# Performance work log

Measured on AMD Instinct MI355X. Metric: run time of the kernel, lower is better.

Reference implementation:

```python
import jax, jax.numpy as jnp
import numpy as np

N = 100000   # num_nodes
E = 1250000  # num_edges
IN = 64
HID = 64
OUT = 64
LN_EPS = 1e-5


def _gcn_conv(x, src, dst, W, b, n):
    # PyG GCNConv: add self-loops, symmetric deg^{-1/2} normalization, then linear.
    h = x @ W  # (N, out)
    deg = jax.ops.segment_sum(jnp.ones(src.shape[0], h.dtype), dst, num_segments=n) + 1.0  # +1 self-loop
    dinv = jax.lax.rsqrt(deg)
    norm = dinv[src] * dinv[dst]  # (E,)
    out = jax.ops.segment_sum(h[src] * norm[:, None], dst, num_segments=n)
    out = out + h * (dinv * dinv)[:, None]  # self-loop message
    return out + b


def _sage_conv(x, src, dst, Wl, bl, Wr, n):
    # PyG SAGEConv(aggr='mean'): lin_l(mean_{j in N(i)} x_j) + lin_r(x_i); bias only in lin_l.
    cnt = jax.ops.segment_sum(jnp.ones(src.shape[0], x.dtype), dst, num_segments=n)
    agg = jax.ops.segment_sum(x[src], dst, num_segments=n) / jnp.maximum(cnt, 1.0)[:, None]
    return agg @ Wl + bl + x @ Wr


def _layer_norm(x, g, b):
    mu = jnp.mean(x, axis=-1, keepdims=True)
    var = jnp.var(x, axis=-1, keepdims=True)
    return (x - mu) * jax.lax.rsqrt(var + LN_EPS) * g + b


def setup_inputs() -> dict:
    key = jax.random.key(0)
    ks = jax.random.split(key, 16)
    def w(k, shape):
        fan_in = shape[0]
        return (jax.random.normal(k, shape, jnp.float32) / np.sqrt(fan_in)).astype(jnp.float32)
    x = jax.random.normal(ks[0], (N, IN), jnp.float32)
    edge_index = jax.random.randint(ks[1], (2, E), 0, N, dtype=jnp.int64)
    return {
        "x": x,
        "edge_index": edge_index,
        "gcn_w1": w(ks[2], (IN, HID)), "gcn_b1": jnp.zeros((HID,), jnp.float32),
        "gcn_w2": w(ks[3], (HID, OUT)), "gcn_b2": jnp.zeros((OUT,), jnp.float32),
        "sage_wl1": w(ks[4], (IN, HID)), "sage_bl1": jnp.zeros((HID,), jnp.float32),
        "sage_wr1": w(ks[5], (IN, HID)),
        "sage_wl2": w(ks[6], (HID, OUT)), "sage_bl2": jnp.zeros((OUT,), jnp.float32),
        "sage_wr2": w(ks[7], (HID, OUT)),
        "gcn_ln_g": jnp.ones((OUT,), jnp.float32), "gcn_ln_b": jnp.zeros((OUT,), jnp.float32),
        "sage_ln_g": jnp.ones((OUT,), jnp.float32), "sage_ln_b": jnp.zeros((OUT,), jnp.float32),
        "proj_w": w(ks[8], (2 * OUT, OUT)), "proj_b": jnp.zeros((OUT,), jnp.float32),
    }


def reference(x, edge_index, gcn_w1, gcn_b1, gcn_w2, gcn_b2,
              sage_wl1, sage_bl1, sage_wr1, sage_wl2, sage_bl2, sage_wr2,
              gcn_ln_g, gcn_ln_b, sage_ln_g, sage_ln_b, proj_w, proj_b):
    src, dst = edge_index[0], edge_index[1]
    n = x.shape[0]
    # GCN branch (dropout p=0 / eval -> identity)
    g = jax.nn.relu(_gcn_conv(x, src, dst, gcn_w1, gcn_b1, n))
    g = _gcn_conv(g, src, dst, gcn_w2, gcn_b2, n)
    # SAGE branch
    s = jax.nn.relu(_sage_conv(x, src, dst, sage_wl1, sage_bl1, sage_wr1, n))
    s = _sage_conv(s, src, dst, sage_wl2, sage_bl2, sage_wr2, n)
    # Norm + projected-concat fusion
    g = _layer_norm(g, gcn_ln_g, gcn_ln_b)
    s = _layer_norm(s, sage_ln_g, sage_ln_b)
    cat = jnp.concatenate([g, s], axis=-1)  # (N, 2*OUT)
    return cat @ proj_w + proj_b
```

## Files before the change

### kernel.cpp

```cpp
#include <hip/hip_runtime.h>


#define SCAN_CHUNK 2048

typedef __attribute__((ext_vector_type(8))) short short8;
typedef __attribute__((ext_vector_type(4))) short short4v;
typedef __attribute__((ext_vector_type(4))) float floatx4;

__device__ __forceinline__ unsigned short f2bf(float f) {
    unsigned int u = __float_as_uint(f);
    unsigned int r = u + 0x7FFFu + ((u >> 16) & 1u);
    return (unsigned short)(r >> 16);
}
__device__ __forceinline__ float bf2f(unsigned short h) {
    return __uint_as_float(((unsigned int)h) << 16);
}

__device__ __forceinline__ unsigned lds_addr(const void* p) {
    return (unsigned)(unsigned long long)(__attribute__((address_space(3))) const char*)p;
}

__device__ __forceinline__ short8 cat44(short4v lo, short4v hi) {
    short8 r;
    r[0] = lo[0]; r[1] = lo[1]; r[2] = lo[2]; r[3] = lo[3];
    r[4] = hi[0]; r[5] = hi[1]; r[6] = hi[2]; r[7] = hi[3];
    return r;
}

template<int NF, int CTB>
__device__ __forceinline__ void tr_read4(unsigned a0, short8 bf[4]) {
    short4v l0, h0, l1, h1, l2, h2, l3, h3;
    asm volatile(
        "ds_read_b64_tr_b16 %0, %8 offset:%9\n\t"
        "ds_read_b64_tr_b16 %1, %8 offset:%10\n\t"
        "ds_read_b64_tr_b16 %2, %8 offset:%11\n\t"
        "ds_read_b64_tr_b16 %3, %8 offset:%12\n\t"
        "ds_read_b64_tr_b16 %4, %8 offset:%13\n\t"
        "ds_read_b64_tr_b16 %5, %8 offset:%14\n\t"
        "ds_read_b64_tr_b16 %6, %8 offset:%15\n\t"
        "ds_read_b64_tr_b16 %7, %8 offset:%16\n\t"
        "s_waitcnt lgkmcnt(0)"
        : "=&v"(l0), "=&v"(h0), "=&v"(l1), "=&v"(h1),
          "=&v"(l2), "=&v"(h2), "=&v"(l3), "=&v"(h3)
        : "v"(a0),
          "i"((0 * NF + CTB + 0) * 128), "i"((1 * NF + CTB + 0) * 128),
          "i"((0 * NF + CTB + 1) * 128), "i"((1 * NF + CTB + 1) * 128),
          "i"((0 * NF + CTB + 2) * 128), "i"((1 * NF + CTB + 2) * 128),
          "i"((0 * NF + CTB + 3) * 128), "i"((1 * NF + CTB + 3) * 128)
        : "memory");
    bf[0] = cat44(l0, h0);
    bf[1] = cat44(l1, h1);
    bf[2] = cat44(l2, h2);
    bf[3] = cat44(l3, h3);
}

__global__ void k_count(const int* __restrict__ ei, int E, int* __restrict__ cnt,
                        int* __restrict__ rank) {
    int i = blockIdx.x * blockDim.x + threadIdx.x;
    int e = i * 4;
    if (e + 4 <= E) {
        int4 d = *(const int4*)&ei[E + e];
        int4 r;
        r.x = atomicAdd(&cnt[d.x], 1);
        r.y = atomicAdd(&cnt[d.y], 1);
        r.z = atomicAdd(&cnt[d.z], 1);
        r.w = atomicAdd(&cnt[d.w], 1);
        *(int4*)&rank[e] = r;
    } else {
        for (int j = e; j < E; ++j) rank[j] = atomicAdd(&cnt[ei[E + j]], 1);
    }
}

__global__ void k_scan_reduce(const int* __restrict__ cnt, int N, int* __restrict__ blockSums) {
    __shared__ int lds[256];
    int base = blockIdx.x * SCAN_CHUNK;
    int t = threadIdx.x;
    int s = 0;
    for (int j = 0; j < 8; ++j) {
        int idx = base + t * 8 + j;
        if (idx < N) s += cnt[idx] + 1;
    }
    lds[t] = s;
    __syncthreads();
    for (int d = 128; d > 0; d >>= 1) {
        if (t < d) lds[t] += lds[t + d];
        __syncthreads();
    }
    if (t == 0) blockSums[blockIdx.x] = lds[0];
}

__global__ void k_scan_spine(int* __restrict__ blockSums, int B) {
    if (threadIdx.x == 0 && blockIdx.x == 0) {
        int run = 0;
        for (int b = 0; b < B; ++b) { int v = blockSums[b]; blockSums[b] = run; run += v; }
    }
}

__global__ void k_scan_write(const int* __restrict__ cnt, int N,
                             const int* __restrict__ blockSums,
                             int* __restrict__ offs, float* __restrict__ dinv) {
    __shared__ int lds[256];
    int base = blockIdx.x * SCAN_CHUNK;
    int t = threadIdx.x;
    int v[8];
    int s = 0;
    for (int j = 0; j < 8; ++j) {
        int idx = base + t * 8 + j;
        v[j] = (idx < N) ? cnt[idx] : 0;
        s += (idx < N) ? v[j] + 1 : 0;
    }
    lds[t] = s;
    __syncthreads();
    for (int d = 1; d < 256; d <<= 1) {
        int x = (t >= d) ? lds[t - d] : 0;
        __syncthreads();
        lds[t] += x;
        __syncthreads();
    }
    int excl = (t == 0) ? 0 : lds[t - 1];
    int run = blockSums[blockIdx.x] + excl;
    for (int j = 0; j < 8; ++j) {
        int idx = base + t * 8 + j;
        if (idx < N) {
            offs[idx] = run;
            run += v[j] + 1;
            dinv[idx] = rsqrtf((float)v[j] + 1.0f);
            if (idx == N - 1) offs[N] = run;
        }
    }
}

__global__ void k_fill(const int* __restrict__ ei, int E, const int* __restrict__ offs,
                       const int* __restrict__ rank, const float* __restrict__ dinv,
                       int* __restrict__ csr, unsigned int* __restrict__ pk, int use_pk) {
    int i = blockIdx.x * blockDim.x + threadIdx.x;
    int e = i * 4;
    if (e + 4 <= E) {
        int4 s = *(const int4*)&ei[e];
        int4 d = *(const int4*)&ei[E + e];
        int4 r = *(const int4*)&rank[e];
        int p0 = offs[d.x] + r.x, p1 = offs[d.y] + r.y;
        int p2 = offs[d.z] + r.z, p3 = offs[d.w] + r.w;
        csr[p0] = s.x; csr[p1] = s.y; csr[p2] = s.z; csr[p3] = s.w;
        if (use_pk) {
            pk[p0] = ((unsigned)(d.x & 15) << 16) | f2bf(dinv[s.x] * dinv[d.x]);
            pk[p1] = ((unsigned)(d.y & 15) << 16) | f2bf(dinv[s.y] * dinv[d.y]);
            pk[p2] = ((unsigned)(d.z & 15) << 16) | f2bf(dinv[s.z] * dinv[d.z]);
            pk[p3] = ((unsigned)(d.w & 15) << 16) | f2bf(dinv[s.w] * dinv[d.w]);
        }
    } else {
        for (int j = e; j < E; ++j) {
            int dd = ei[E + j];
            int p = offs[dd] + rank[j];
            csr[p] = ei[j];
            if (use_pk) pk[p] = ((unsigned)(dd & 15) << 16) | f2bf(dinv[ei[j]] * dinv[dd]);
        }
    }
}

__global__ void k_self(const int* __restrict__ offs, const int* __restrict__ cnt,
                       const float* __restrict__ dinv,
                       int* __restrict__ csr, unsigned int* __restrict__ pk, int N) {
    int i = blockIdx.x * blockDim.x + threadIdx.x;
    if (i < N) {
        int pos = offs[i] + cnt[i];
        float di = dinv[i];
        csr[pos] = i;
        pk[pos] = ((unsigned)(i & 15) << 16) | (1u << 20) | f2bf(di * di);
    }
}

__global__ void k_xtobf16(const float* __restrict__ x, unsigned short* __restrict__ xb, int total) {
    int i = blockIdx.x * blockDim.x + threadIdx.x;
    int e = i * 8;
    if (e + 8 <= total) {
        float4 a = *(const float4*)&x[e];
        float4 b = *(const float4*)&x[e + 4];
        short8 o;
        o[0] = (short)f2bf(a.x); o[1] = (short)f2bf(a.y);
        o[2] = (short)f2bf(a.z); o[3] = (short)f2bf(a.w);
        o[4] = (short)f2bf(b.x); o[5] = (short)f2bf(b.y);
        o[6] = (short)f2bf(b.z); o[7] = (short)f2bf(b.w);
        *(short8*)&xb[e] = o;
    } else {
        for (int j = e; j < total; ++j) xb[j] = f2bf(x[j]);
    }
}

template<int ROWSH>
__launch_bounds__(256)
__global__ void k_gatherM(const unsigned short* __restrict__ feat,
                          const int* __restrict__ csr,
                          const unsigned int* __restrict__ pk,
                          const int* __restrict__ offs, const int* __restrict__ cnt,
                          unsigned short* __restrict__ agg, int N) {
    constexpr int NF = ROWSH / 16;
    constexpr int EPP = (NF == 8) ? 4 : 8;
    constexpr int PASSES = 32 / EPP;

    __shared__ unsigned short sbuf[4 * 32 * ROWSH];

    const int lane = threadIdx.x & 63;
    const int wave = threadIdx.x >> 6;
    const int base = blockIdx.x * 64 + wave * 16;
    if (base >= N) return;

    unsigned short* wb = &sbuf[wave * 32 * ROWSH];
    const unsigned wboff = lds_addr(wb);
    const int q = lane >> 4;
    const int d16 = lane & 15;

    const int parity = lane & 1;
    const int ei_low = (lane >> 1) & 3;
    const int sf_sub = (lane >> 3) & (NF - 1);
    const int ei_high = (NF == 8) ? 0 : (lane >> 5);
    const int ei = ei_high * 4 + ei_low;
    const int sf = sf_sub * 16 + parity * 8;

    const int elo = offs[base];
    const int ehi = offs[min(base + 16, N)];

    floatx4 accg[4], accs[4];
#pragma unroll
    for (int i = 0; i < 4; ++i) {
        accg[i] = floatx4{0.f, 0.f, 0.f, 0.f};
        accs[i] = floatx4{0.f, 0.f, 0.f, 0.f};
    }

    const unsigned a0 = wboff + (unsigned)(q * 2 * NF) * 128u + (unsigned)d16 * 8u;

    if (elo < ehi) {
        const int emax = ehi - 1;

        auto meta = [&](int k0, int& csrv, unsigned& pkv) {
            int idx = k0 + lane;
            int idc = idx <= emax ? idx : emax;
            csrv = csr[idc];
            pkv = (idx < ehi) ? pk[idx] : 0x00100000u;
        };
        auto issue = [&](short8* stg, int csrv) {
#pragma unroll
            for (int p = 0; p < PASSES; ++p) {
                int src = __shfl(csrv, p * EPP + ei, 64);
                stg[p] = *(const short8*)&feat[(size_t)src * ROWSH + sf];
            }
        };
        auto process = [&](const short8* stg, unsigned pkv) {
#pragma unroll
            for (int p = 0; p < PASSES; ++p)
                *(short8*)&wb[p * 512 + lane * 8] = stg[p];
            short8 aG, aS;
#pragma unroll
            for (int j = 0; j < 8; ++j) {
                unsigned u = (unsigned)__shfl((int)pkv, q * 8 + j, 64);
                unsigned hi = u >> 16;
                bool match = (int)(hi & 15u) == d16;
                aG[j] = match ? (short)(u & 0xFFFFu) : (short)0;
                aS[j] = (match && !(hi & 16u)) ? (short)0x3F80 : (short)0;
            }
            asm volatile("s_waitcnt lgkmcnt(0)" ::: "memory");
            __builtin_amdgcn_sched_barrier(0);
            short8 bG[4];
            tr_read4<NF, 0>(a0, bG);
#pragma unroll
            for (int ct = 0; ct < 4; ++ct)
                accg[ct] = __builtin_amdgcn_mfma_f32_16x16x32_bf16(aG, bG[ct], accg[ct], 0, 0, 0);
            if constexpr (NF == 8) {
                short8 bS[4];
                tr_read4<NF, 4>(a0, bS);
#pragma unroll
                for (int ct = 0; ct < 4; ++ct)
                    accs[ct] = __builtin_amdgcn_mfma_f32_16x16x32_bf16(aS, bS[ct], accs[ct], 0, 0, 0);
            } else {
#pragma unroll
                for (int ct = 0; ct < 4; ++ct)
                    accs[ct] = __builtin_amdgcn_mfma_f32_16x16x32_bf16(aS, bG[ct], accs[ct], 0, 0, 0);
            }
        };

        int csrvA, csrvN;
        unsigned pkvA, pkvB, pkvN;
        short8 sA[PASSES], sB[PASSES];

        meta(elo, csrvA, pkvA);
        issue(sA, csrvA);
        meta(elo + 32, csrvN, pkvN);

        int k0 = elo;
        while (true) {
            issue(sB, csrvN);
            pkvB = pkvN;
            meta(k0 + 64, csrvN, pkvN);
            process(sA, pkvA);
            k0 += 32;
            if (k0 >= ehi) break;
            issue(sA, csrvN);
            pkvA = pkvN;
            meta(k0 + 64, csrvN, pkvN);
            process(sB, pkvB);
            k0 += 32;
            if (k0 >= ehi) break;
        }
    }

#pragma unroll
    for (int r = 0; r < 4; ++r) {
        int node = base + q * 4 + r;
        if (node < N) {
            float rn = 1.0f / fmaxf((float)cnt[node], 1.0f);
#pragma unroll
            for (int ct = 0; ct < 4; ++ct) {
                agg[(size_t)node * 128 + ct * 16 + d16]      = f2bf(accg[ct][r]);
                agg[(size_t)node * 128 + 64 + ct * 16 + d16] = f2bf(accs[ct][r] * rn);
            }
        }
    }
}

__device__ __forceinline__ void xor_reduce8(float4& a, float4& b) {
    a.x += __shfl_xor(a.x, 16, 64); a.y += __shfl_xor(a.y, 16, 64);
    a.z += __shfl_xor(a.z, 16, 64); a.w += __shfl_xor(a.w, 16, 64);
    b.x += __shfl_xor(b.x, 16, 64); b.y += __shfl_xor(b.y, 16, 64);
    b.z += __shfl_xor(b.z, 16, 64); b.w += __shfl_xor(b.w, 16, 64);
    a.x += __shfl_xor(a.x, 32, 64); a.y += __shfl_xor(a.y, 32, 64);
    a.z += __shfl_xor(a.z, 32, 64); a.w += __shfl_xor(a.w, 32, 64);
    b.x += __shfl_xor(b.x, 32, 64); b.y += __shfl_xor(b.y, 32, 64);
    b.z += __shfl_xor(b.z, 32, 64); b.w += __shfl_xor(b.w, 32, 64);
}

__device__ __forceinline__ float red16(float v) {
    v += __shfl_xor(v, 1, 64);
    v += __shfl_xor(v, 2, 64);
    v += __shfl_xor(v, 4, 64);
    v += __shfl_xor(v, 8, 64);
    return v;
}

__global__ void k_gather1_f32(const float* __restrict__ x, const int* __restrict__ csr,
                              const int* __restrict__ offs, const int* __restrict__ cnt,
                              const float* __restrict__ dinv,
                              unsigned short* __restrict__ agg, int N) {
    int lane = threadIdx.x & 63;
    int wave = threadIdx.x >> 6;
    int node = blockIdx.x * 4 + wave;
    if (node >= N) return;
    int c = lane & 15, grp = lane >> 4;

    int st = offs[node];
    int cn = cnt[node];
    float di = dinv[node];

    float4 aA = {0.f, 0.f, 0.f, 0.f}, aB = {0.f, 0.f, 0.f, 0.f};
    for (int e = 0; e < cn; e += 8) {
        int i0 = e + grp, i1 = e + 4 + grp;
        float m0 = (i0 < cn) ? 1.f : 0.f;
        float m1 = (i1 < cn) ? 1.f : 0.f;
        int s0 = csr[st + (i0 < cn ? i0 : cn - 1)];
        int s1 = csr[st + (i1 < cn ? i1 : cn - 1)];
        float w0 = m0 * dinv[s0];
        float w1 = m1 * dinv[s1];
        float4 v0 = *(const float4*)&x[(size_t)s0 * 64 + 4 * c];
        float4 v1 = *(const float4*)&x[(size_t)s1 * 64 + 4 * c];
        aA.x += w0 * v0.x + w1 * v1.x; aA.y += w0 * v0.y + w1 * v1.y;
        aA.z += w0 * v0.z + w1 * v1.z; aA.w += w0 * v0.w + w1 * v1.w;
        aB.x += m0 * v0.x + m1 * v1.x; aB.y += m0 * v0.y + m1 * v1.y;
        aB.z += m0 * v0.z + m1 * v1.z; aB.w += m0 * v0.w + m1 * v1.w;
    }
    xor_reduce8(aA, aB);

    if (grp == 0) {
        float4 sq = *(const float4*)&x[(size_t)node * 64 + 4 * c];
        float d2 = di * di;
        ushort4 o;
        o.x = f2bf(di * aA.x + d2 * sq.x); o.y = f2bf(di * aA.y + d2 * sq.y);
        o.z = f2bf(di * aA.z + d2 * sq.z); o.w = f2bf(di * aA.w + d2 * sq.w);
        *(ushort4*)&agg[(size_t)node * 128 + 4 * c] = o;
    } else if (grp == 1) {
        float rn = 1.0f / fmaxf((float)cn, 1.0f);
        ushort4 o;
        o.x = f2bf(aB.x * rn); o.y = f2bf(aB.y * rn);
        o.z = f2bf(aB.z * rn); o.w = f2bf(aB.w * rn);
        *(ushort4*)&agg[(size_t)node * 128 + 64 + 4 * c] = o;
    }
}

__global__ void k_gather2(const unsigned short* __restrict__ gs, const int* __restrict__ csr,
                          const int* __restrict__ offs, const int* __restrict__ cnt,
                          const float* __restrict__ dinv,
                          unsigned short* __restrict__ agg, int N) {
    int lane = threadIdx.x & 63;
    int wave = threadIdx.x >> 6;
    int node = blockIdx.x * 4 + wave;
    if (node >= N) return;
    int c = lane & 15, grp = lane >> 4;

    int st = offs[node];
    int cn = cnt[node];
    float di = dinv[node];

    float4 aC = {0.f, 0.f, 0.f, 0.f}, aD = {0.f, 0.f, 0.f, 0.f};
    for (int e = 0; e < cn; e += 8) {
        int i0 = e + grp, i1 = e + 4 + grp;
        float m0 = (i0 < cn) ? 1.f : 0.f;
        float m1 = (i1 < cn) ? 1.f : 0.f;
        int s0 = csr[st + (i0 < cn ? i0 : cn - 1)];
        int s1 = csr[st + (i1 < cn ? i1 : cn - 1)];
        float w0 = m0 * dinv[s0];
        float w1 = m1 * dinv[s1];
        const unsigned short* p0 = gs + (size_t)s0 * 128 + 4 * c;
        const unsigned short* p1 = gs + (size_t)s1 * 128 + 4 * c;
        ushort4 g0u = *(const ushort4*)p0;
        ushort4 g1u = *(const ushort4*)p1;
        ushort4 t0u = *(const ushort4*)(p0 + 64);
        ushort4 t1u = *(const ushort4*)(p1 + 64);
        aC.x += w0 * bf2f(g0u.x) + w1 * bf2f(g1u.x);
        aC.y += w0 * bf2f(g0u.y) + w1 * bf2f(g1u.y);
        aC.z += w0 * bf2f(g0u.z) + w1 * bf2f(g1u.z);
        aC.w += w0 * bf2f(g0u.w) + w1 * bf2f(g1u.w);
        aD.x += m0 * bf2f(t0u.x) + m1 * bf2f(t1u.x);
        aD.y += m0 * bf2f(t0u.y) + m1 * bf2f(t1u.y);
        aD.z += m0 * bf2f(t0u.z) + m1 * bf2f(t1u.z);
        aD.w += m0 * bf2f(t0u.w) + m1 * bf2f(t1u.w);
    }
    xor_reduce8(aC, aD);

    if (grp == 0) {
        ushort4 su = *(const ushort4*)&gs[(size_t)node * 128 + 4 * c];
        float d2 = di * di;
        ushort4 o;
        o.x = f2bf(di * aC.x + d2 * bf2f(su.x));
        o.y = f2bf(di * aC.y + d2 * bf2f(su.y));
        o.z = f2bf(di * aC.z + d2 * bf2f(su.z));
        o.w = f2bf(di * aC.w + d2 * bf2f(su.w));
        *(ushort4*)&agg[(size_t)node * 128 + 4 * c] = o;
    } else if (grp == 1) {
        float rn = 1.0f / fmaxf((float)cn, 1.0f);
        ushort4 o;
        o.x = f2bf(aD.x * rn); o.y = f2bf(aD.y * rn);
        o.z = f2bf(aD.z * rn); o.w = f2bf(aD.w * rn);
        *(ushort4*)&agg[(size_t)node * 128 + 64 + 4 * c] = o;
    }
}

__launch_bounds__(512, 1)
__global__ void k_gemm1(const unsigned short* __restrict__ agg,
                        const unsigned short* __restrict__ xb,
                        const float* __restrict__ xf, int use_xb,
                        const float* __restrict__ W1, const float* __restrict__ b1,
                        const float* __restrict__ Wl1, const float* __restrict__ bl1,
                        const float* __restrict__ Wr1,
                        unsigned short* __restrict__ buf1, int N) {
    alignas(16) __shared__ unsigned short sW[3][4096];
    int t = threadIdx.x;
    for (int i = t; i < 1536; i += 512) {
        int m = i >> 9;
        int rem = i & 511;
        int f = rem >> 6;
        int L = rem & 63;
        int kb = (f >> 2) * 32 + (L >> 4) * 8;
        int o = (f & 3) * 16 + (L & 15);
        const float* Wsrc = (m == 0) ? W1 : (m == 1) ? Wl1 : Wr1;
        unsigned short* dst = &sW[m][f * 512 + L * 8];
        #pragma unroll
        for (int j = 0; j < 8; ++j) dst[j] = f2bf(Wsrc[(kb + j) * 64 + o]);
    }
    __syncthreads();

    int lane = t & 63;
    int wave = t >> 6;
    int quad = lane >> 4;
    int n16 = lane & 15;
    int base = blockIdx.x * 128 + wave * 16;
    if (base >= N) return;

    int nm = base + n16;
    if (nm >= N) nm = N - 1;
    const unsigned short* ar = agg + (size_t)nm * 128;

    {
        short8 a0 = *(const short8*)(ar + quad * 8);
        short8 a1 = *(const short8*)(ar + 32 + quad * 8);
        floatx4 g0 = {0.f, 0.f, 0.f, 0.f}, g1 = g0, g2 = g0, g3 = g0;
        g0 = __builtin_amdgcn_mfma_f32_16x16x32_bf16(a0, *(const short8*)&sW[0][0 * 512 + lane * 8], g0, 0, 0, 0);
        g0 = __builtin_amdgcn_mfma_f32_16x16x32_bf16(a1, *(const short8*)&sW[0][4 * 512 + lane * 8], g0, 0, 0, 0);
        g1 = __builtin_amdgcn_mfma_f32_16x16x32_bf16(a0, *(const short8*)&sW[0][1 * 512 + lane * 8], g1, 0, 0, 0);
        g1 = __builtin_amdgcn_mfma_f32_16x16x32_bf16(a1, *(const short8*)&sW[0][5 * 512 + lane * 8], g1, 0, 0, 0);
        g2 = __builtin_amdgcn_mfma_f32_16x16x32_bf16(a0, *(const short8*)&sW[0][2 * 512 + lane * 8], g2, 0, 0, 0);
        g2 = __builtin_amdgcn_mfma_f32_16x16x32_bf16(a1, *(const short8*)&sW[0][6 * 512 + lane * 8], g2, 0, 0, 0);
        g3 = __builtin_amdgcn_mfma_f32_16x16x32_bf16(a0, *(const short8*)&sW[0][3 * 512 + lane * 8], g3, 0, 0, 0);
        g3 = __builtin_amdgcn_mfma_f32_16x16x32_bf16(a1, *(const short8*)&sW[0][7 * 512 + lane * 8], g3, 0, 0, 0);
        floatx4 gt[4] = {g0, g1, g2, g3};
        #pragma unroll
        for (int nt = 0; nt < 4; ++nt) {
            float bg = b1[nt * 16 + n16];
            #pragma unroll
            for (int r = 0; r < 4; ++r) {
                int node = base + quad * 4 + r;
                if (node < N)
                    buf1[(size_t)node * 128 + nt * 16 + n16] = f2bf(fmaxf(gt[nt][r] + bg, 0.f));
            }
        }
    }

    {
        short8 a0 = *(const short8*)(ar + 64 + quad * 8);
        short8 a1 = *(const short8*)(ar + 96 + quad * 8);
        short8 ax0, ax1;
        if (use_xb) {
            ax0 = *(const short8*)&xb[(size_t)nm * 64 + quad * 8];
            ax1 = *(const short8*)&xb[(size_t)nm * 64 + 32 + quad * 8];
        } else {
            float4 xq0 = *(const float4*)&xf[(size_t)nm * 64 + quad * 8];
            float4 xq1 = *(const float4*)&xf[(size_t)nm * 64 + quad * 8 + 4];
            float4 xq2 = *(const float4*)&xf[(size_t)nm * 64 + 32 + quad * 8];
            float4 xq3 = *(const float4*)&xf[(size_t)nm * 64 + 32 + quad * 8 + 4];
            ax0[0] = (short)f2bf(xq0.x); ax0[1] = (short)f2bf(xq0.y);
            ax0[2] = (short)f2bf(xq0.z); ax0[3] = (short)f2bf(xq0.w);
            ax0[4] = (short)f2bf(xq1.x); ax0[5] = (short)f2bf(xq1.y);
            ax0[6] = (short)f2bf(xq1.z); ax0[7] = (short)f2bf(xq1.w);
            ax1[0] = (short)f2bf(xq2.x); ax1[1] = (short)f2bf(xq2.y);
            ax1[2] = (short)f2bf(xq2.z); ax1[3] = (short)f2bf(xq2.w);
            ax1[4] = (short)f2bf(xq3.x); ax1[5] = (short)f2bf(xq3.y);
            ax1[6] = (short)f2bf(xq3.z); ax1[7] = (short)f2bf(xq3.w);
        }

        floatx4 s0 = {0.f, 0.f, 0.f, 0.f}, s1 = s0, s2 = s0, s3 = s0;
        s0 = __builtin_amdgcn_mfma_f32_16x16x32_bf16(a0, *(const short8*)&sW[1][0 * 512 + lane * 8], s0, 0, 0, 0);
        s0 = __builtin_amdgcn_mfma_f32_16x16x32_bf16(a1, *(const short8*)&sW[1][4 * 512 + lane * 8], s0, 0, 0, 0);
        s0 = __builtin_amdgcn_mfma_f32_16x16x32_bf16(ax0, *(const short8*)&sW[2][0 * 512 + lane * 8], s0, 0, 0, 0);
        s0 = __builtin_amdgcn_mfma_f32_16x16x32_bf16(ax1, *(const short8*)&sW[2][4 * 512 + lane * 8], s0, 0, 0, 0);
        s1 = __builtin_amdgcn_mfma_f32_16x16x32_bf16(a0, *(const short8*)&sW[1][1 * 512 + lane * 8], s1, 0, 0, 0);
        s1 = __builtin_amdgcn_mfma_f32_16x16x32_bf16(a1, *(const short8*)&sW[1][5 * 512 + lane * 8], s1, 0, 0, 0);
        s1 = __builtin_amdgcn_mfma_f32_16x16x32_bf16(ax0, *(const short8*)&sW[2][1 * 512 + lane * 8], s1, 0, 0, 0);
        s1 = __builtin_amdgcn_mfma_f32_16x16x32_bf16(ax1, *(const short8*)&sW[2][5 * 512 + lane * 8], s1, 0, 0, 0);
        s2 = __builtin_amdgcn_mfma_f32_16x16x32_bf16(a0, *(const short8*)&sW[1][2 * 512 + lane * 8], s2, 0, 0, 0);
        s2 = __builtin_amdgcn_mfma_f32_16x16x32_bf16(a1, *(const short8*)&sW[1][6 * 512 + lane * 8], s2, 0, 0, 0);
        s2 = __builtin_amdgcn_mfma_f32_16x16x32_bf16(ax0, *(const short8*)&sW[2][2 * 512 + lane * 8], s2, 0, 0, 0);
        s2 = __builtin_amdgcn_mfma_f32_16x16x32_bf16(ax1, *(const short8*)&sW[2][6 * 512 + lane * 8], s2, 0, 0, 0);
        s3 = __builtin_amdgcn_mfma_f32_16x16x32_bf16(a0, *(const short8*)&sW[1][3 * 512 + lane * 8], s3, 0, 0, 0);
        s3 = __builtin_amdgcn_mfma_f32_16x16x32_bf16(a1, *(const short8*)&sW[1][7 * 512 + lane * 8], s3, 0, 0, 0);
        s3 = __builtin_amdgcn_mfma_f32_16x16x32_bf16(ax0, *(const short8*)&sW[2][3 * 512 + lane * 8], s3, 0, 0, 0);
        s3 = __builtin_amdgcn_mfma_f32_16x16x32_bf16(ax1, *(const short8*)&sW[2][7 * 512 + lane * 8], s3, 0, 0, 0);
        floatx4 stl[4] = {s0, s1, s2, s3};
        #pragma unroll
        for (int nt = 0; nt < 4; ++nt) {
            float bs = bl1[nt * 16 + n16];
            #pragma unroll
            for (int r = 0; r < 4; ++r) {
                int node = base + quad * 4 + r;
                if (node < N)
                    buf1[(size_t)node * 128 + 64 + nt * 16 + n16] = f2bf(fmaxf(stl[nt][r] + bs, 0.f));
            }
        }
    }
}

__launch_bounds__(512, 1)
__global__ void k_gemm2(const unsigned short* __restrict__ agg,
                        const unsigned short* __restrict__ buf1,
                        const float* __restrict__ W2, const float* __restrict__ b2,
                        const float* __restrict__ Wl2, const float* __restrict__ bl2,
                        const float* __restrict__ Wr2,
                        const float* __restrict__ lngG, const float* __restrict__ lnbG,
                        const float* __restrict__ lngS, const float* __restrict__ lnbS,
                        const float* __restrict__ Pw, const float* __restrict__ Pb,
                        float* __restrict__ out, int N) {
    alignas(16) __shared__ unsigned short sW[3][4096];
    alignas(16) __shared__ unsigned short sP[8192];
    alignas(16) __shared__ unsigned short sT[8][16 * 132];
    int t = threadIdx.x;
    for (int i = t; i < 1536; i += 512) {
        int m = i >> 9;
        int rem = i & 511;
        int f = rem >> 6;
        int L = rem & 63;
        int kb = (f >> 2) * 32 + (L >> 4) * 8;
        int o = (f & 3) * 16 + (L & 15);
        const float* Wsrc = (m == 0) ? W2 : (m == 1) ? Wl2 : Wr2;
        unsigned short* dst = &sW[m][f * 512 + L * 8];
        #pragma unroll
        for (int j = 0; j < 8; ++j) dst[j] = f2bf(Wsrc[(kb + j) * 64 + o]);
    }
    for (int i = t; i < 1024; i += 512) {
        int f = i >> 6;
        int L = i & 63;
        int kb = (f >> 2) * 32 + (L >> 4) * 8;
        int o = (f & 3) * 16 + (L & 15);
        unsigned short* dst = &sP[f * 512 + L * 8];
        #pragma unroll
        for (int j = 0; j < 8; ++j) dst[j] = f2bf(Pw[(kb + j) * 64 + o]);
    }
    __syncthreads();

    int lane = t & 63;
    int wave = t >> 6;
    int quad = lane >> 4;
    int n16 = lane & 15;
    int base = blockIdx.x * 128 + wave * 16;
    if (base >= N) return;
    int nm = base + n16;
    if (nm >= N) nm = N - 1;
    const unsigned short* ar = agg + (size_t)nm * 128;
    const unsigned short* br = buf1 + (size_t)nm * 128;
    unsigned short* tw = &sT[wave][0];

    {
        short8 a0 = *(const short8*)(ar + quad * 8);
        short8 a1 = *(const short8*)(ar + 32 + quad * 8);
        floatx4 c0 = {0.f, 0.f, 0.f, 0.f}, c1 = c0, c2 = c0, c3 = c0;
        c0 = __builtin_amdgcn_mfma_f32_16x16x32_bf16(a0, *(const short8*)&sW[0][0 * 512 + lane * 8], c0, 0, 0, 0);
        c0 = __builtin_amdgcn_mfma_f32_16x16x32_bf16(a1, *(const short8*)&sW[0][4 * 512 + lane * 8], c0, 0, 0, 0);
        c1 = __builtin_amdgcn_mfma_f32_16x16x32_bf16(a0, *(const short8*)&sW[0][1 * 512 + lane * 8], c1, 0, 0, 0);
        c1 = __builtin_amdgcn_mfma_f32_16x16x32_bf16(a1, *(const short8*)&sW[0][5 * 512 + lane * 8], c1, 0, 0, 0);
        c2 = __builtin_amdgcn_mfma_f32_16x16x32_bf16(a0, *(const short8*)&sW[0][2 * 512 + lane * 8], c2, 0, 0, 0);
        c2 = __builtin_amdgcn_mfma_f32_16x16x32_bf16(a1, *(const short8*)&sW[0][6 * 512 + lane * 8], c2, 0, 0, 0);
        c3 = __builtin_amdgcn_mfma_f32_16x16x32_bf16(a0, *(const short8*)&sW[0][3 * 512 + lane * 8], c3, 0, 0, 0);
        c3 = __builtin_amdgcn_mfma_f32_16x16x32_bf16(a1, *(const short8*)&sW[0][7 * 512 + lane * 8], c3, 0, 0, 0);

        float bv0 = b2[n16], bv1 = b2[16 + n16], bv2 = b2[32 + n16], bv3 = b2[48 + n16];
        float gv0 = lngG[n16], gv1 = lngG[16 + n16], gv2 = lngG[32 + n16], gv3 = lngG[48 + n16];
        float ev0 = lnbG[n16], ev1 = lnbG[16 + n16], ev2 = lnbG[32 + n16], ev3 = lnbG[48 + n16];
        #pragma unroll
        for (int r = 0; r < 4; ++r) {
            float z0 = c0[r] + bv0, z1 = c1[r] + bv1, z2 = c2[r] + bv2, z3 = c3[r] + bv3;
            float s = red16(z0 + z1 + z2 + z3);
            float q = red16(z0 * z0 + z1 * z1 + z2 * z2 + z3 * z3);
            float mu = s * (1.0f / 64.0f);
            float var = fmaxf(q * (1.0f / 64.0f) - mu * mu, 0.0f);
            float rs = rsqrtf(var + 1e-5f);
            unsigned short* row = tw + (quad * 4 + r) * 132;
            row[n16]      = f2bf((z0 - mu) * rs * gv0 + ev0);
            row[16 + n16] = f2bf((z1 - mu) * rs * gv1 + ev1);
            row[32 + n16] = f2bf((z2 - mu) * rs * gv2 + ev2);
            row[48 + n16] = f2bf((z3 - mu) * rs * gv3 + ev3);
        }
    }

    {
        short8 a0 = *(const short8*)(ar + 64 + quad * 8);
        short8 a1 = *(const short8*)(ar + 96 + quad * 8);
        short8 v0 = *(const short8*)(br + 64 + quad * 8);
        short8 v1 = *(const short8*)(br + 96 + quad * 8);
        floatx4 c0 = {0.f, 0.f, 0.f, 0.f}, c1 = c0, c2 = c0, c3 = c0;
        c0 = __builtin_amdgcn_mfma_f32_16x16x32_bf16(a0, *(const short8*)&sW[1][0 * 512 + lane * 8], c0, 0, 0, 0);
        c0 = __builtin_amdgcn_mfma_f32_16x16x32_bf16(a1, *(const short8*)&sW[1][4 * 512 + lane * 8], c0, 0, 0, 0);
        c0 = __builtin_amdgcn_mfma_f32_16x16x32_bf16(v0, *(const short8*)&sW[2][0 * 512 + lane * 8], c0, 0, 0, 0);
        c0 = __builtin_amdgcn_mfma_f32_16x16x32_bf16(v1, *(const short8*)&sW[2][4 * 512 + lane * 8], c0, 0, 0, 0);
        c1 = __builtin_amdgcn_mfma_f32_16x16x32_bf16(a0, *(const short8*)&sW[1][1 * 512 + lane * 8], c1, 0, 0, 0);
        c1 = __builtin_amdgcn_mfma_f32_16x16x32_bf16(a1, *(const short8*)&sW[1][5 * 512 + lane * 8], c1, 0, 0, 0);
        c1 = __builtin_amdgcn_mfma_f32_16x16x32_bf16(v0, *(const short8*)&sW[2][1 * 512 + lane * 8], c1, 0, 0, 0);
        c1 = __builtin_amdgcn_mfma_f32_16x16x32_bf16(v1, *(const short8*)&sW[2][5 * 512 + lane * 8], c1, 0, 0, 0);
        c2 = __builtin_amdgcn_mfma_f32_16x16x32_bf16(a0, *(const short8*)&sW[1][2 * 512 + lane * 8], c2, 0, 0, 0);
        c2 = __builtin_amdgcn_mfma_f32_16x16x32_bf16(a1, *(const short8*)&sW[1][6 * 512 + lane * 8], c2, 0, 0, 0);
        c2 = __builtin_amdgcn_mfma_f32_16x16x32_bf16(v0, *(const short8*)&sW[2][2 * 512 + lane * 8], c2, 0, 0, 0);
        c2 = __builtin_amdgcn_mfma_f32_16x16x32_bf16(v1, *(const short8*)&sW[2][6 * 512 + lane * 8], c2, 0, 0, 0);
        c3 = __builtin_amdgcn_mfma_f32_16x16x32_bf16(a0, *(const short8*)&sW[1][3 * 512 + lane * 8], c3, 0, 0, 0);
        c3 = __builtin_amdgcn_mfma_f32_16x16x32_bf16(a1, *(const short8*)&sW[1][7 * 512 + lane * 8], c3, 0, 0, 0);
        c3 = __builtin_amdgcn_mfma_f32_16x16x32_bf16(v0, *(const short8*)&sW[2][3 * 512 + lane * 8], c3, 0, 0, 0);
        c3 = __builtin_amdgcn_mfma_f32_16x16x32_bf16(v1, *(const short8*)&sW[2][7 * 512 + lane * 8], c3, 0, 0, 0);

        float bv0 = bl2[n16], bv1 = bl2[16 + n16], bv2 = bl2[32 + n16], bv3 = bl2[48 + n16];
        float gv0 = lngS[n16], gv1 = lngS[16 + n16], gv2 = lngS[32 + n16], gv3 = lngS[48 + n16];
        float ev0 = lnbS[n16], ev1 = lnbS[16 + n16], ev2 = lnbS[32 + n16], ev3 = lnbS[48 + n16];
        #pragma unroll
        for (int r = 0; r < 4; ++r) {
            float z0 = c0[r] + bv0, z1 = c1[r] + bv1, z2 = c2[r] + bv2, z3 = c3[r] + bv3;
            float s = red16(z0 + z1 + z2 + z3);
            float q = red16(z0 * z0 + z1 * z1 + z2 * z2 + z3 * z3);
            float mu = s * (1.0f / 64.0f);
            float var = fmaxf(q * (1.0f / 64.0f) - mu * mu, 0.0f);
            float rs = rsqrtf(var + 1e-5f);
            unsigned short* row = tw + (quad * 4 + r) * 132 + 64;
            row[n16]      = f2bf((z0 - mu) * rs * gv0 + ev0);
            row[16 + n16] = f2bf((z1 - mu) * rs * gv1 + ev1);
            row[32 + n16] = f2bf((z2 - mu) * rs * gv2 + ev2);
            row[48 + n16] = f2bf((z3 - mu) * rs * gv3 + ev3);
        }
    }

    floatx4 o0 = {0.f, 0.f, 0.f, 0.f}, o1 = o0, o2 = o0, o3 = o0;
    #pragma unroll
    for (int ks = 0; ks < 4; ++ks) {
        const unsigned short* ap = tw + n16 * 132 + ks * 32 + quad * 8;
        short4v lo = *(const short4v*)ap;
        short4v hi = *(const short4v*)(ap + 4);
        short8 af;
        af[0] = lo[0]; af[1] = lo[1]; af[2] = lo[2]; af[3] = lo[3];
        af[4] = hi[0]; af[5] = hi[1]; af[6] = hi[2]; af[7] = hi[3];
        o0 = __builtin_amdgcn_mfma_f32_16x16x32_bf16(af, *(const short8*)&sP[(ks * 4 + 0) * 512 + lane * 8], o0, 0, 0, 0);
        o1 = __builtin_amdgcn_mfma_f32_16x16x32_bf16(af, *(const short8*)&sP[(ks * 4 + 1) * 512 + lane * 8], o1, 0, 0, 0);
        o2 = __builtin_amdgcn_mfma_f32_16x16x32_bf16(af, *(const short8*)&sP[(ks * 4 + 2) * 512 + lane * 8], o2, 0, 0, 0);
        o3 = __builtin_amdgcn_mfma_f32_16x16x32_bf16(af, *(const short8*)&sP[(ks * 4 + 3) * 512 + lane * 8], o3, 0, 0, 0);
    }
    float p0 = Pb[n16], p1 = Pb[16 + n16], p2 = Pb[32 + n16], p3 = Pb[48 + n16];
    floatx4 ot[4] = {o0, o1, o2, o3};
    float pv[4] = {p0, p1, p2, p3};
    #pragma unroll
    for (int nt = 0; nt < 4; ++nt) {
        #pragma unroll
        for (int r = 0; r < 4; ++r) {
            int node = base + quad * 4 + r;
            if (node < N) out[(size_t)node * 64 + nt * 16 + n16] = ot[nt][r] + pv[nt];
        }
    }
}

extern "C" void kernel_launch(void* const* d_in, const int* in_sizes, int n_in,
                              void* d_out, int out_size, void* d_ws, size_t ws_size,
                              hipStream_t stream) {
    const float* x        = (const float*)d_in[0];
    const int*   ei       = (const int*)d_in[1];
    const float* gcn_w1   = (const float*)d_in[2];
    const float* gcn_b1   = (const float*)d_in[3];
    const float* gcn_w2   = (const float*)d_in[4];
    const float* gcn_b2   = (const float*)d_in[5];
    const float* sage_wl1 = (const float*)d_in[6];
    const float* sage_bl1 = (const float*)d_in[7];
    const float* sage_wr1 = (const float*)d_in[8];
    const float* sage_wl2 = (const float*)d_in[9];
    const float* sage_bl2 = (const float*)d_in[10];
    const float* sage_wr2 = (const float*)d_in[11];
    const float* gcn_ln_g = (const float*)d_in[12];
    const float* gcn_ln_b = (const float*)d_in[13];
    const float* sage_ln_g = (const float*)d_in[14];
    const float* sage_ln_b = (const float*)d_in[15];
    const float* proj_w   = (const float*)d_in[16];
    const float* proj_b   = (const float*)d_in[17];
    float* out = (float*)d_out;

    const int N = in_sizes[0] / 64;
    const int E = in_sizes[1] / 2;
    const int B = (N + SCAN_CHUNK - 1) / SCAN_CHUNK;

    char* w = (char*)d_ws;
    size_t off = 0;
    auto alloc = [&](size_t bytes) -> void* {
        void* p = w + off;
        off = (off + bytes + 255) & ~(size_t)255;
        return p;
    };
    int*            cnt       = (int*)alloc((size_t)N * 4);
    int*            offs      = (int*)alloc((size_t)(N + 1) * 4);
    float*          dinv      = (float*)alloc((size_t)N * 4);
    int*            blockSums = (int*)alloc((size_t)(B + 1) * 4);
    int*            csr       = (int*)alloc((size_t)(E + N + 64) * 4);
    unsigned short* agg       = (unsigned short*)alloc((size_t)N * 128 * 2);
    unsigned short* buf1      = (unsigned short*)alloc((size_t)N * 128 * 2);
    size_t off_nonew = off;
    unsigned int*   pk        = (unsigned int*)alloc((size_t)(E + N + 64) * 4);
    unsigned short* xb        = (unsigned short*)alloc((size_t)N * 64 * 2);
    int use_new = (off <= ws_size) ? 1 : 0;
    if (!use_new) off = off_nonew;
    int* rank = (int*)agg;
    (void)n_in; (void)out_size;

    hipMemsetAsync(cnt, 0, (size_t)N * 4, stream);

    int e4Blocks = ((E + 3) / 4 + 255) / 256;
    k_count<<<e4Blocks, 256, 0, stream>>>(ei, E, cnt, rank);
    k_scan_reduce<<<B, 256, 0, stream>>>(cnt, N, blockSums);
    k_scan_spine<<<1, 64, 0, stream>>>(blockSums, B);
    k_scan_write<<<B, 256, 0, stream>>>(cnt, N, blockSums, offs, dinv);
    k_fill<<<e4Blocks, 256, 0, stream>>>(ei, E, offs, rank, dinv, csr, pk, use_new);

    if (use_new) {
        k_self<<<(N + 255) / 256, 256, 0, stream>>>(offs, cnt, dinv, csr, pk, N);
        int xBlocks = ((N * 64 + 7) / 8 + 255) / 256;
        k_xtobf16<<<xBlocks, 256, 0, stream>>>(x, xb, N * 64);
        k_gatherM<64><<<(N + 63) / 64, 256, 0, stream>>>(xb, csr, pk, offs, cnt, agg, N);
        k_gemm1<<<(N + 127) / 128, 512, 0, stream>>>(agg, xb, x, 1, gcn_w1, gcn_b1,
                                                     sage_wl1, sage_bl1, sage_wr1, buf1, N);
        k_gatherM<128><<<(N + 63) / 64, 256, 0, stream>>>(buf1, csr, pk, offs, cnt, agg, N);
    } else {
        k_gather1_f32<<<(N + 3) / 4, 256, 0, stream>>>(x, csr, offs, cnt, dinv, agg, N);
        k_gemm1<<<(N + 127) / 128, 512, 0, stream>>>(agg, xb, x, 0, gcn_w1, gcn_b1,
                                                     sage_wl1, sage_bl1, sage_wr1, buf1, N);
        k_gather2<<<(N + 3) / 4, 256, 0, stream>>>(buf1, csr, offs, cnt, dinv, agg, N);
    }
    k_gemm2<<<(N + 127) / 128, 512, 0, stream>>>(agg, buf1, gcn_w2, gcn_b2,
                                                 sage_wl2, sage_bl2, sage_wr2,
                                                 gcn_ln_g, gcn_ln_b, sage_ln_g, sage_ln_b,
                                                 proj_w, proj_b, out, N);
}
```

Baseline: 345.6 us.

## Stream gathered neighbor rows directly into double-buffered LDS via global_load_lds

The MFMA-based neighbor gather now copies neighbor feature rows straight from global memory into LDS using global_load_lds, instead of loading them into registers and then writing them to LDS. It double-buffers two LDS slots per wave, prefetches the first 256 edges of CSR/packed metadata up front, and waits with partial vmcnt so the next chunk's loads overlap the current chunk's MFMAs. Blocks shrink to 128 threads covering 32 nodes, which changes occupancy and grid size. The intent is to cut staging-register pressure and VGPR-to-LDS write traffic. In exchange it depends on the order in which vmcnt counters retire, and loads more metadata per wave up front.

Result: slower. 361.8 us (+4.7%).

```diff
diff --git a/kernel.cpp b/kernel.cpp
--- a/kernel.cpp
+++ b/kernel.cpp
@@ -18,6 +18,19 @@
 
 __device__ __forceinline__ unsigned lds_addr(const void* p) {
     return (unsigned)(unsigned long long)(__attribute__((address_space(3))) const char*)p;
+}
+
+__device__ __forceinline__ void gload_lds16(const void* g, void* l) {
+    __builtin_amdgcn_global_load_lds(
+        (const __attribute__((address_space(1))) unsigned int*)g,
+        (__attribute__((address_space(3))) unsigned int*)l, 16, 0, 0);
+}
+
+template<int NN>
+__device__ __forceinline__ void wait_vmcnt() {
+    if constexpr (NN == 8)      asm volatile("s_waitcnt vmcnt(8)" ::: "memory");
+    else if constexpr (NN == 4) asm volatile("s_waitcnt vmcnt(4)" ::: "memory");
+    else                        asm volatile("s_waitcnt vmcnt(0)" ::: "memory");
 }
 
 __device__ __forceinline__ short8 cat44(short4v lo, short4v hi) {
@@ -188,25 +201,24 @@
 }
 
 template<int ROWSH>
-__launch_bounds__(256)
+__launch_bounds__(128)
 __global__ void k_gatherM(const unsigned short* __restrict__ feat,
                           const int* __restrict__ csr,
                           const unsigned int* __restrict__ pk,
                           const int* __restrict__ offs, const int* __restrict__ cnt,
                           unsigned short* __restrict__ agg, int N) {
     constexpr int NF = ROWSH / 16;
-    constexpr int EPP = (NF == 8) ? 4 : 8;
+    constexpr int LPR = ROWSH / 8;
+    constexpr int EPP = 64 / LPR;
     constexpr int PASSES = 32 / EPP;
 
-    __shared__ unsigned short sbuf[4 * 32 * ROWSH];
+    __shared__ unsigned short sbuf[2][2][32 * ROWSH];
 
     const int lane = threadIdx.x & 63;
-    const int wave = threadIdx.x >> 6;
-    const int base = blockIdx.x * 64 + wave * 16;
+    const int wv = threadIdx.x >> 6;
+    const int base = blockIdx.x * 32 + wv * 16;
     if (base >= N) return;
 
-    unsigned short* wb = &sbuf[wave * 32 * ROWSH];
-    const unsigned wboff = lds_addr(wb);
     const int q = lane >> 4;
     const int d16 = lane & 15;
 
@@ -214,11 +226,32 @@
     const int ei_low = (lane >> 1) & 3;
     const int sf_sub = (lane >> 3) & (NF - 1);
     const int ei_high = (NF == 8) ? 0 : (lane >> 5);
-    const int ei = ei_high * 4 + ei_low;
+    const int eid = ei_high * 4 + ei_low;
     const int sf = sf_sub * 16 + parity * 8;
 
     const int elo = offs[base];
     const int ehi = offs[min(base + 16, N)];
+    const int emax = ehi - 1;
+    const int nch = (ehi - elo + 31) >> 5;
+
+    int cM0, cM1, cM2, cM3;
+    unsigned pM0, pM1, pM2, pM3;
+    {
+        int i0 = elo + lane;
+        int i1 = i0 + 64, i2 = i0 + 128, i3 = i0 + 192;
+        cM0 = csr[i0 <= emax ? i0 : emax];
+        cM1 = csr[i1 <= emax ? i1 : emax];
+        cM2 = csr[i2 <= emax ? i2 : emax];
+        cM3 = csr[i3 <= emax ? i3 : emax];
+        unsigned t0 = pk[i0 <= emax ? i0 : emax];
+        unsigned t1 = pk[i1 <= emax ? i1 : emax];
+        unsigned t2 = pk[i2 <= emax ? i2 : emax];
+        unsigned t3 = pk[i3 <= emax ? i3 : emax];
+        pM0 = (i0 < ehi) ? t0 : 0x00100000u;
+        pM1 = (i1 < ehi) ? t1 : 0x00100000u;
+        pM2 = (i2 < ehi) ? t2 : 0x00100000u;
+        pM3 = (i3 < ehi) ? t3 : 0x00100000u;
+    }
 
     floatx4 accg[4], accs[4];
 #pragma unroll
@@ -227,80 +260,81 @@
         accs[i] = floatx4{0.f, 0.f, 0.f, 0.f};
     }
 
-    const unsigned a0 = wboff + (unsigned)(q * 2 * NF) * 128u + (unsigned)d16 * 8u;
-
-    if (elo < ehi) {
-        const int emax = ehi - 1;
-
-        auto meta = [&](int k0, int& csrv, unsigned& pkv) {
-            int idx = k0 + lane;
+    unsigned short* wb0 = &sbuf[wv][0][0];
+    unsigned short* wb1 = &sbuf[wv][1][0];
+    const unsigned a0base = (unsigned)(q * 2 * NF) * 128u + (unsigned)d16 * 8u;
+    const unsigned a0_0 = lds_addr(wb0) + a0base;
+    const unsigned a0_1 = lds_addr(wb1) + a0base;
+
+    auto getmeta = [&](int c, int& cv, unsigned& pv, int& wofs) {
+        int rc = c >> 1;
+        if (rc < 4) {
+            wofs = (c & 1) << 5;
+            cv = (rc == 0) ? cM0 : (rc == 1) ? cM1 : (rc == 2) ? cM2 : cM3;
+            pv = (rc == 0) ? pM0 : (rc == 1) ? pM1 : (rc == 2) ? pM2 : pM3;
+        } else {
+            int idx = elo + (c << 5) + lane;
             int idc = idx <= emax ? idx : emax;
-            csrv = csr[idc];
-            pkv = (idx < ehi) ? pk[idx] : 0x00100000u;
-        };
-        auto issue = [&](short8* stg, int csrv) {
+            cv = csr[idc];
+            unsigned t = pk[idc];
+            pv = (idx < ehi) ? t : 0x00100000u;
+            wofs = 0;
+        }
+    };
+
+    auto issue = [&](unsigned short* dst, int cv, int wofs) {
 #pragma unroll
-            for (int p = 0; p < PASSES; ++p) {
-                int src = __shfl(csrv, p * EPP + ei, 64);
-                stg[p] = *(const short8*)&feat[(size_t)src * ROWSH + sf];
-            }
-        };
-        auto process = [&](const short8* stg, unsigned pkv) {
+        for (int p = 0; p < PASSES; ++p) {
+            int src = __shfl(cv, wofs + p * EPP + eid, 64);
+            gload_lds16(&feat[(size_t)src * ROWSH + sf], dst + p * 512);
+        }
+        __builtin_amdgcn_sched_barrier(0);
+    };
+
+    int cv; unsigned pv; int wofs;
+    getmeta(0, cv, pv, wofs);
+    issue(wb0, cv, wofs);
+    unsigned pvC = pv; int wofsC = wofs;
+
+    int cur = 0;
+    for (int c = 0; c < nch; ++c) {
+        bool pf = (c + 1 < nch);
+        if (pf) {
+            getmeta(c + 1, cv, pv, wofs);
+            issue(cur ? wb0 : wb1, cv, wofs);
+        }
+        short8 aG, aS;
 #pragma unroll
-            for (int p = 0; p < PASSES; ++p)
-                *(short8*)&wb[p * 512 + lane * 8] = stg[p];
-            short8 aG, aS;
+        for (int j = 0; j < 8; ++j) {
+            unsigned u = (unsigned)__shfl((int)pvC, wofsC + q * 8 + j, 64);
+            unsigned hi = u >> 16;
+            bool match = (int)(hi & 15u) == d16;
+            aG[j] = match ? (short)(u & 0xFFFFu) : (short)0;
+            aS[j] = (match && !(hi & 16u)) ? (short)0x3F80 : (short)0;
+        }
+        if (pf) wait_vmcnt<PASSES>();
+        else    wait_vmcnt<0>();
+        __builtin_amdgcn_sched_barrier(0);
+
+        const unsigned a0 = cur ? a0_1 : a0_0;
+        short8 bG[4];
+        tr_read4<NF, 0>(a0, bG);
 #pragma unroll
-            for (int j = 0; j < 8; ++j) {
-                unsigned u = (unsigned)__shfl((int)pkv, q * 8 + j, 64);
-                unsigned hi = u >> 16;
-                bool match = (int)(hi & 15u) == d16;
-                aG[j] = match ? (short)(u & 0xFFFFu) : (short)0;
-                aS[j] = (match && !(hi & 16u)) ? (short)0x3F80 : (short)0;
-            }
-            asm volatile("s_waitcnt lgkmcnt(0)" ::: "memory");
-            __builtin_amdgcn_sched_barrier(0);
-            short8 bG[4];
-            tr_read4<NF, 0>(a0, bG);
+        for (int ct = 0; ct < 4; ++ct)
+            accg[ct] = __builtin_amdgcn_mfma_f32_16x16x32_bf16(aG, bG[ct], accg[ct], 0, 0, 0);
+        if constexpr (NF == 8) {
+            short8 bS[4];
+            tr_read4<NF, 4>(a0, bS);
 #pragma unroll
             for (int ct = 0; ct < 4; ++ct)
-                accg[ct] = __builtin_amdgcn_mfma_f32_16x16x32_bf16(aG, bG[ct], accg[ct], 0, 0, 0);
-            if constexpr (NF == 8) {
-                short8 bS[4];
-                tr_read4<NF, 4>(a0, bS);
+                accs[ct] = __builtin_amdgcn_mfma_f32_16x16x32_bf16(aS, bS[ct], accs[ct], 0, 0, 0);
+        } else {
 #pragma unroll
-                for (int ct = 0; ct < 4; ++ct)
-                    accs[ct] = __builtin_amdgcn_mfma_f32_16x16x32_bf16(aS, bS[ct], accs[ct], 0, 0, 0);
-            } else {
-#pragma unroll
-                for (int ct = 0; ct < 4; ++ct)
-                    accs[ct] = __builtin_amdgcn_mfma_f32_16x16x32_bf16(aS, bG[ct], accs[ct], 0, 0, 0);
-            }
-        };
-
-        int csrvA, csrvN;
-        unsigned pkvA, pkvB, pkvN;
-        short8 sA[PASSES], sB[PASSES];
-
-        meta(elo, csrvA, pkvA);
-        issue(sA, csrvA);
-        meta(elo + 32, csrvN, pkvN);
-
-        int k0 = elo;
-        while (true) {
-            issue(sB, csrvN);
-            pkvB = pkvN;
-            meta(k0 + 64, csrvN, pkvN);
-            process(sA, pkvA);
-            k0 += 32;
-            if (k0 >= ehi) break;
-            issue(sA, csrvN);
-            pkvA = pkvN;
-            meta(k0 + 64, csrvN, pkvN);
-            process(sB, pkvB);
-            k0 += 32;
-            if (k0 >= ehi) break;
-        }
+            for (int ct = 0; ct < 4; ++ct)
+                accs[ct] = __builtin_amdgcn_mfma_f32_16x16x32_bf16(aS, bG[ct], accs[ct], 0, 0, 0);
+        }
+        pvC = pv; wofsC = wofs;
+        cur ^= 1;
     }
 
 #pragma unroll
@@ -767,10 +801,10 @@
         k_self<<<(N + 255) / 256, 256, 0, stream>>>(offs, cnt, dinv, csr, pk, N);
         int xBlocks = ((N * 64 + 7) / 8 + 255) / 256;
         k_xtobf16<<<xBlocks, 256, 0, stream>>>(x, xb, N * 64);
-        k_gatherM<64><<<(N + 63) / 64, 256, 0, stream>>>(xb, csr, pk, offs, cnt, agg, N);
+        k_gatherM<64><<<(N + 31) / 32, 128, 0, stream>>>(xb, csr, pk, offs, cnt, agg, N);
         k_gemm1<<<(N + 127) / 128, 512, 0, stream>>>(agg, xb, x, 1, gcn_w1, gcn_b1,
                                                      sage_wl1, sage_bl1, sage_wr1, buf1, N);
-        k_gatherM<128><<<(N + 63) / 64, 256, 0, stream>>>(buf1, csr, pk, offs, cnt, agg, N);
+        k_gatherM<128><<<(N + 31) / 32, 128, 0, stream>>>(buf1, csr, pk, offs, cnt, agg, N);
     } else {
         k_gather1_f32<<<(N + 3) / 4, 256, 0, stream>>>(x, csr, offs, cnt, dinv, agg, N);
         k_gemm1<<<(N + 127) / 128, 512, 0, stream>>>(agg, xb, x, 0, gcn_w1, gcn_b1,
```
